# Optimization experiments

Hardware: AMD Instinct MI355X
Metric: run time of the kernel (lower is better)

The kernel has to match this reference:

```python
import jax, jax.numpy as jnp
import numpy as np

N = 100_000   # nodes
E = 1_250_000 # edges
D = 64        # node feature dim
H = 64        # hidden_channels
C = 10        # num_classes
G = 128       # graphs in batch


def setup_inputs() -> dict:
    key = jax.random.key(0)
    ks = jax.random.split(key, 12)
    x = jax.random.normal(ks[0], (N, D), dtype=jnp.float32)
    edge_index = jax.random.randint(ks[1], (2, E), 0, N, dtype=jnp.int64)
    batch = jnp.sort(jax.random.randint(ks[2], (N,), 0, G, dtype=jnp.int64))
    s = lambda fan_in: 1.0 / np.sqrt(fan_in)
    W1 = jax.random.normal(ks[3], (D, H), dtype=jnp.float32) * s(D)
    b1 = jnp.zeros((H,), dtype=jnp.float32)
    W2 = jax.random.normal(ks[4], (H, H), dtype=jnp.float32) * s(H)
    b2 = jnp.zeros((H,), dtype=jnp.float32)
    W3 = jax.random.normal(ks[5], (H, H), dtype=jnp.float32) * s(H)
    b3 = jnp.zeros((H,), dtype=jnp.float32)
    Wl = jax.random.normal(ks[6], (H, C), dtype=jnp.float32) * s(H)
    bl = jnp.zeros((C,), dtype=jnp.float32)
    return {"x": x, "edge_index": edge_index, "batch": batch,
            "W1": W1, "b1": b1, "W2": W2, "b2": b2,
            "W3": W3, "b3": b3, "Wl": Wl, "bl": bl}


def _gcn_conv(h, W, b, src, dst, norm, n_nodes):
    # GCNConv: out[i] = sum_{e: dst(e)=i} norm_e * (h @ W)[src(e)] + b
    h = h @ W
    msg = h[src] * norm[:, None]                       # [E+N, H]
    return jax.ops.segment_sum(msg, dst, num_segments=n_nodes) + b


def reference(x, edge_index, batch, W1, b1, W2, b2, W3, b3, Wl, bl):
    x = x.astype(jnp.float32)
    ei = edge_index.astype(jnp.int64)
    # add self-loops (as PyG gcn_norm does by default)
    loop = jnp.arange(N, dtype=ei.dtype)
    src = jnp.concatenate([ei[0], loop])
    dst = jnp.concatenate([ei[1], loop])
    # symmetric normalization: deg over targets (in-degree incl. self-loops)
    deg = jax.ops.segment_sum(jnp.ones_like(src, dtype=jnp.float32), dst,
                              num_segments=N)
    dinv = jnp.where(deg > 0, jax.lax.rsqrt(jnp.maximum(deg, 1.0)), 0.0)
    norm = dinv[src] * dinv[dst]                       # [E+N]

    h = jax.nn.relu(_gcn_conv(x, W1, b1, src, dst, norm, N))
    h = jax.nn.relu(_gcn_conv(h, W2, b2, src, dst, norm, N))
    h = _gcn_conv(h, W3, b3, src, dst, norm, N)

    # global_mean_pool over graph ids
    ones = jnp.ones((N,), dtype=jnp.float32)
    counts = jax.ops.segment_sum(ones, batch, num_segments=G)
    sums = jax.ops.segment_sum(h, batch, num_segments=G)
    pooled = sums / jnp.maximum(counts, 1.0)[:, None]  # [G, H]

    # dropout is identity in eval mode
    return pooled @ Wl + bl                            # [G, C]
```

## Files before the change

### kernel.cpp

```cpp
#include <hip/hip_runtime.h>
#include <hip/hip_bf16.h>


#define BSHIFT 7
#define BNODES (1 << BSHIFT)
#define EPB    8192
#define MAXDEG 8192
#define MAXBUCKET 32768

typedef __attribute__((ext_vector_type(8))) short bf16x8;
typedef __attribute__((ext_vector_type(4))) float f32x4;

#define KAS __attribute__((address_space(4)))

template <typename T>
__device__ __forceinline__ const KAS T* kptr(const T* p) {
    return (const KAS T*)(unsigned long long)p;
}

__device__ __forceinline__ void atomAddF(float* p, float v) {
#if defined(__gfx90a__) || defined(__gfx940__) || defined(__gfx941__) || defined(__gfx942__) || defined(__gfx950__)
    unsafeAtomicAdd(p, v);
#else
    atomicAdd(p, v);
#endif
}

__device__ __forceinline__ unsigned short f2bf(float x) {
    unsigned u = __float_as_uint(x);
    u += 0x7FFFu + ((u >> 16) & 1u);
    return (unsigned short)(u >> 16);
}
__device__ __forceinline__ float bf2f(unsigned short b) {
    return __uint_as_float((unsigned)b << 16);
}

__global__ __launch_bounds__(256)
void k_bhist(const int* __restrict__ dst, int* __restrict__ cnt_all,
             int nE, int nBuckets, int binBlocks,
             const float* __restrict__ W1, const float* __restrict__ W2,
             const float* __restrict__ W3, unsigned short* __restrict__ Wt,
             float* __restrict__ pool, int poolN) {
    if (blockIdx.x >= binBlocks) {
        int li = blockIdx.x - binBlocks;
        if (li < 3) {
            const float* W = (li == 0) ? W1 : ((li == 1) ? W2 : W3);
            unsigned short* o = Wt + li * 4096;
            for (int idx = threadIdx.x; idx < 4096; idx += 256) {
                int h = idx >> 6, k = idx & 63;
                o[idx] = f2bf(W[k * 64 + h]);
            }
        } else {
            for (int i = threadIdx.x; i < poolN; i += 256) pool[i] = 0.f;
        }
        return;
    }
    __shared__ int cnt[1024];
    const int t = threadIdx.x;
    const int blk = blockIdx.x * EPB;
    for (int b = t; b < nBuckets; b += 256) cnt[b] = 0;
    __syncthreads();
#pragma unroll 4
    for (int i = 0; i < EPB / 256; i++) {
        int e = blk + i * 256 + t;
        if (e < nE) atomicAdd(&cnt[dst[e] >> BSHIFT], 1);
    }
    __syncthreads();
    for (int b = t; b < nBuckets; b += 256)
        cnt_all[(size_t)blockIdx.x * nBuckets + b] = cnt[b];
}

__global__ __launch_bounds__(256)
void k_colscan(int* __restrict__ cnt_all, int* __restrict__ bcnt,
               int nBlocks, int nBuckets) {
    const int lane = threadIdx.x & 63;
    const int b = blockIdx.x * 4 + (threadIdx.x >> 6);
    if (b >= nBuckets) return;
    int running = 0;
    for (int c = 0; c < nBlocks; c += 64) {
        int blk = c + lane;
        int v = (blk < nBlocks) ? cnt_all[(size_t)blk * nBuckets + b] : 0;
        int incl = v;
#pragma unroll
        for (int off = 1; off < 64; off <<= 1) {
            int tv = __shfl_up(incl, off);
            if (lane >= off) incl += tv;
        }
        if (blk < nBlocks) cnt_all[(size_t)blk * nBuckets + b] = running + (incl - v);
        running += __shfl(incl, 63);
    }
    if (lane == 0) bcnt[b] = running;
}

__global__ void k_bscan(const int* __restrict__ bcnt, int* __restrict__ bbase,
                        int nb, int nE) {
    __shared__ int s[256];
    const int t = threadIdx.x;
    const int base = t * 4;
    int v0 = (base + 0 < nb) ? bcnt[base + 0] : 0;
    int v1 = (base + 1 < nb) ? bcnt[base + 1] : 0;
    int v2 = (base + 2 < nb) ? bcnt[base + 2] : 0;
    int v3 = (base + 3 < nb) ? bcnt[base + 3] : 0;
    int tsum = v0 + v1 + v2 + v3;
    s[t] = tsum;
    __syncthreads();
    for (int off = 1; off < 256; off <<= 1) {
        int val = 0;
        if (t >= off) val = s[t - off];
        __syncthreads();
        if (t >= off) s[t] += val;
        __syncthreads();
    }
    int excl = s[t] - tsum;
    if (base + 0 < nb) bbase[base + 0] = excl;
    if (base + 1 < nb) bbase[base + 1] = excl + v0;
    if (base + 2 < nb) bbase[base + 2] = excl + v0 + v1;
    if (base + 3 < nb) bbase[base + 3] = excl + v0 + v1 + v2;
    if (t == 0) bbase[nb] = nE;
}

__global__ __launch_bounds__(256)
void k_bucket(const int* __restrict__ src, const int* __restrict__ dst,
              const int* __restrict__ bbase, const int* __restrict__ cnt_all,
              int* __restrict__ staging, int nE, int nBuckets) {
    __shared__ int cnt[1024];
    __shared__ int lbase[1024];
    const int t = threadIdx.x;
    const int blk = blockIdx.x * EPB;

    for (int b = t; b < nBuckets; b += 256) {
        lbase[b] = bbase[b] + cnt_all[(size_t)blockIdx.x * nBuckets + b];
        cnt[b] = 0;
    }
    __syncthreads();
#pragma unroll 4
    for (int i = 0; i < EPB / 256; i++) {
        int e = blk + i * 256 + t;
        if (e < nE) {
            int s0 = src[e], d0 = dst[e];
            int b = d0 >> BSHIFT;
            int off = atomicAdd(&cnt[b], 1);
            int pos = lbase[b] + off;
            if ((unsigned)pos < (unsigned)nE)
                staging[pos] = (s0 << BSHIFT) | (d0 & (BNODES - 1));
        }
    }
}

__global__ __launch_bounds__(256)
void k_sort(const int* __restrict__ staging, const int* __restrict__ bbase,
            int* __restrict__ csr_s, int* __restrict__ rowptr,
            int* __restrict__ rowend, float* __restrict__ dinv,
            int n, int nE) {
    __shared__ int c[BNODES];
    __shared__ int sc[BNODES];
    __shared__ int cur[BNODES];
    const int t = threadIdx.x;
    const int b = blockIdx.x;
    const int node0 = b << BSHIFT;

    int seg0 = bbase[b];
    int seg1 = bbase[b + 1];
    seg0 = max(0, min(seg0, nE));
    seg1 = max(seg0, min(seg1, nE));
    seg1 = min(seg1, seg0 + MAXBUCKET);

    if (t < BNODES) c[t] = 0;
    __syncthreads();
    for (int e = seg0 + t; e < seg1; e += 256)
        atomicAdd(&c[staging[e] & (BNODES - 1)], 1);
    __syncthreads();
    if (t < BNODES) sc[t] = c[t];
    __syncthreads();
    for (int off = 1; off < BNODES; off <<= 1) {
        int v = 0;
        if (t >= off && t < BNODES) v = sc[t - off];
        __syncthreads();
        if (t >= off && t < BNODES) sc[t] += v;
        __syncthreads();
    }
    if (t < BNODES) {
        int excl = sc[t] - c[t];
        cur[t] = excl;
        int node = node0 + t;
        if (node < n) {
            rowptr[node] = seg0 + excl;
            rowend[node] = seg0 + excl + c[t];
            dinv[node]   = rsqrtf((float)c[t] + 1.0f);
        }
    }
    __syncthreads();
    for (int e = seg0 + t; e < seg1; e += 256) {
        int p = staging[e];
        int l = p & (BNODES - 1);
        int pos = seg0 + atomicAdd(&cur[l], 1);
        if ((unsigned)pos < (unsigned)nE)
            csr_s[pos] = ((unsigned)p) >> BSHIFT;
    }
}

template<bool RELU, typename AT>
__device__ __forceinline__
void gemm_body(int bid, const AT* __restrict__ in,
               const unsigned short* __restrict__ Wt,
               const float* __restrict__ bias,
               unsigned short* __restrict__ out, int n) {
    const int lane = threadIdx.x & 63;
    const int wid  = threadIdx.x >> 6;
    const int col  = lane & 15;
    const int quad = lane >> 4;
    const int node0w = bid * 64 + wid * 16;
    const int nodeA  = node0w + col;
    const bool validA = nodeA < n;

    f32x4 zero4 = {0.f, 0.f, 0.f, 0.f};
    f32x4 acc0 = zero4, acc1 = zero4, acc2 = zero4, acc3 = zero4;

#pragma unroll
    for (int ks = 0; ks < 64; ks += 32) {
        const int kb = ks + quad * 8;
        float a[8];
        if constexpr (sizeof(AT) == 4) {
            float4 a0 = make_float4(0.f, 0.f, 0.f, 0.f);
            float4 a1 = make_float4(0.f, 0.f, 0.f, 0.f);
            if (validA) {
                a0 = *(const float4*)((const float*)in + (size_t)nodeA * 64 + kb);
                a1 = *(const float4*)((const float*)in + (size_t)nodeA * 64 + kb + 4);
            }
            a[0] = a0.x; a[1] = a0.y; a[2] = a0.z; a[3] = a0.w;
            a[4] = a1.x; a[5] = a1.y; a[6] = a1.z; a[7] = a1.w;
        } else {
            ushort4 h0 = make_ushort4(0, 0, 0, 0), h1 = make_ushort4(0, 0, 0, 0);
            if (validA) {
                h0 = *(const ushort4*)((const unsigned short*)in + (size_t)nodeA * 64 + kb);
                h1 = *(const ushort4*)((const unsigned short*)in + (size_t)nodeA * 64 + kb + 4);
            }
            a[0] = bf2f(h0.x); a[1] = bf2f(h0.y); a[2] = bf2f(h0.z); a[3] = bf2f(h0.w);
            a[4] = bf2f(h1.x); a[5] = bf2f(h1.y); a[6] = bf2f(h1.z); a[7] = bf2f(h1.w);
        }
        if (RELU) {
#pragma unroll
            for (int i = 0; i < 8; i++) a[i] = fmaxf(a[i] + bias[kb + i], 0.f);
        }
        bf16x8 af;
#pragma unroll
        for (int i = 0; i < 8; i++) af[i] = (short)f2bf(a[i]);

        const bf16x8 b0f = *(const bf16x8*)(Wt + ((0 * 16 + col) * 64 + kb));
        const bf16x8 b1f = *(const bf16x8*)(Wt + ((1 * 16 + col) * 64 + kb));
        const bf16x8 b2f = *(const bf16x8*)(Wt + ((2 * 16 + col) * 64 + kb));
        const bf16x8 b3f = *(const bf16x8*)(Wt + ((3 * 16 + col) * 64 + kb));
        acc0 = __builtin_amdgcn_mfma_f32_16x16x32_bf16(af, b0f, acc0, 0, 0, 0);
        acc1 = __builtin_amdgcn_mfma_f32_16x16x32_bf16(af, b1f, acc1, 0, 0, 0);
        acc2 = __builtin_amdgcn_mfma_f32_16x16x32_bf16(af, b2f, acc2, 0, 0, 0);
        acc3 = __builtin_amdgcn_mfma_f32_16x16x32_bf16(af, b3f, acc3, 0, 0, 0);
    }

#pragma unroll
    for (int r = 0; r < 4; r++) {
        int nn = node0w + quad * 4 + r;
        if (nn < n) {
            size_t base = (size_t)nn * 64 + col;
            out[base +  0] = f2bf(acc0[r]);
            out[base + 16] = f2bf(acc1[r]);
            out[base + 32] = f2bf(acc2[r]);
            out[base + 48] = f2bf(acc3[r]);
        }
    }
}

template<bool RELU, typename AT>
__global__ __launch_bounds__(256)
void k_gemm(const AT* __restrict__ in, const unsigned short* __restrict__ Wt,
            const float* __restrict__ bias, unsigned short* __restrict__ out, int n) {
    gemm_body<RELU, AT>(blockIdx.x, in, Wt, bias, out, n);
}

__global__ __launch_bounds__(256)
void k_wfgemm1(const int* __restrict__ csr_s, const float* __restrict__ dinv,
               float* __restrict__ csr_w, int nE, int n, int wfB,
               const float* __restrict__ x, const unsigned short* __restrict__ Wt,
               unsigned short* __restrict__ hW) {
    if (blockIdx.x < wfB) {
        int e = blockIdx.x * 256 + threadIdx.x;
        if (e < nE) {
            int s = csr_s[e];
            s = max(0, min(s, n - 1));
            csr_w[e] = dinv[s];
        }
        return;
    }
    gemm_body<false, float>(blockIdx.x - wfB, x, Wt, nullptr, hW, n);
}

template<int LAYER>
__global__ __launch_bounds__(256)
void k_agg(const unsigned short* __restrict__ hW, const int* __restrict__ rowptr,
           const int* __restrict__ rowend, const int* __restrict__ csr_s,
           const float* __restrict__ csr_w, const float* __restrict__ dinv,
           unsigned short* __restrict__ aggb, int n, int nE) {
    const int lane = threadIdx.x & 63;
    const int wid  = threadIdx.x >> 6;
    const int node = blockIdx.x * 4 + wid;
    if (node >= n) return;

    int rowA = __builtin_amdgcn_readfirstlane(rowptr[node]);
    int endA = __builtin_amdgcn_readfirstlane(rowend[node]);
    rowA = max(0, min(rowA, nE)); endA = max(rowA, min(endA, nE));
    endA = min(endA, rowA + MAXDEG);
    const float diA = __uint_as_float(
        __builtin_amdgcn_readfirstlane(__float_as_uint(dinv[node])));

    float acc0 = diA * bf2f(hW[(size_t)node * 64 + lane]);
    float acc1 = 0.f, acc2 = 0.f, acc3 = 0.f;
    const int nm1 = n - 1;

    for (int b = rowA; b < endA; b += 16) {
        const KAS int*   sp = kptr(csr_s + b);
        const KAS float* wp = kptr(csr_w + b);
        const int rem = endA - b;

        int   sidx[16];
        float w[16];
#pragma unroll
        for (int j = 0; j < 16; j++) {
            int s = sp[j];
            s = max(0, min(s, nm1));
            sidx[j] = (j < rem) ? s : 0;
            w[j]    = (j < rem) ? wp[j] : 0.f;
        }
        float h[16];
#pragma unroll
        for (int j = 0; j < 16; j++)
            h[j] = bf2f(hW[(size_t)sidx[j] * 64 + lane]);
#pragma unroll
        for (int j = 0; j < 16; j += 4) {
            acc0 += w[j]     * h[j];
            acc1 += w[j + 1] * h[j + 1];
            acc2 += w[j + 2] * h[j + 2];
            acc3 += w[j + 3] * h[j + 3];
        }
    }
    float r = diA * ((acc0 + acc1) + (acc2 + acc3));
    aggb[(size_t)node * 64 + lane] = f2bf(r);
}

__global__ void k_pool(const unsigned short* __restrict__ aggb,
                       const int* __restrict__ batch,
                       float* __restrict__ pool, float* __restrict__ cnt, int n) {
    const int lane = threadIdx.x;
    const int base = blockIdx.x * 64;
    int g_cur = -1, run = 0;
    float acc = 0.f;
    for (int j = 0; j < 64; j++) {
        int node = base + j;
        if (node >= n) break;
        int g = batch[node];
        if (g != g_cur) {
            if (g_cur >= 0) {
                atomAddF(&pool[g_cur * 64 + lane], acc);
                if (lane == 0) atomAddF(&cnt[g_cur], (float)run);
            }
            g_cur = g; acc = 0.f; run = 0;
        }
        acc += bf2f(aggb[(size_t)node * 64 + lane]);
        run++;
    }
    if (g_cur >= 0) {
        atomAddF(&pool[g_cur * 64 + lane], acc);
        if (lane == 0) atomAddF(&cnt[g_cur], (float)run);
    }
}

__global__ void k_final(const float* __restrict__ pool, const float* __restrict__ cnt,
                        const float* __restrict__ b3, const float* __restrict__ Wl,
                        const float* __restrict__ bl, float* __restrict__ out) {
    __shared__ float s[64];
    const int g = blockIdx.x, t = threadIdx.x;
    float c = fmaxf(cnt[g], 1.0f);
    s[t] = pool[g * 64 + t] / c + b3[t];
    __syncthreads();
    if (t < 10) {
        float acc = bl[t];
#pragma unroll
        for (int k = 0; k < 64; k++) acc += s[k] * Wl[k * 10 + t];
        out[g * 10 + t] = acc;
    }
}

extern "C" void kernel_launch(void* const* d_in, const int* in_sizes, int n_in,
                              void* d_out, int out_size, void* d_ws, size_t ws_size,
                              hipStream_t stream) {
    const float* x   = (const float*)d_in[0];
    const int*   ei  = (const int*)d_in[1];
    const int*   bat = (const int*)d_in[2];
    const float* W1  = (const float*)d_in[3];
    const float* b1  = (const float*)d_in[4];
    const float* W2  = (const float*)d_in[5];
    const float* b2  = (const float*)d_in[6];
    const float* W3  = (const float*)d_in[7];
    const float* b3  = (const float*)d_in[8];
    const float* Wl  = (const float*)d_in[9];
    const float* bl  = (const float*)d_in[10];
    float* out = (float*)d_out;

    const int N_ = in_sizes[0] / 64;
    const int E_ = in_sizes[1] / 2;
    const int G_ = out_size / 10;
    const int NB_ = (N_ + BNODES - 1) >> BSHIFT;
    const int bin_blocks = (E_ + EPB - 1) / EPB;

    char* p = (char*)d_ws;
    int*   staging = (int*)p;   p += (size_t)E_ * 4;
    int*   csr_s  = (int*)p;    p += (size_t)E_ * 4;
    float* csr_w  = (float*)p;  p += (size_t)E_ * 4;
    unsigned short* aggb = (unsigned short*)p; p += (size_t)N_ * 64 * 2;
    unsigned short* hW   = (unsigned short*)p; p += (size_t)N_ * 64 * 2;
    float* dinv   = (float*)p;  p += (size_t)N_ * 4;
    int*   rowptr = (int*)p;    p += (size_t)N_ * 4;
    int*   rowend = (int*)p;    p += (size_t)N_ * 4;
    float* pool   = (float*)p;  p += (size_t)G_ * 64 * 4;
    float* cnt    = (float*)p;  p += (size_t)G_ * 4;
    unsigned short* Wt = (unsigned short*)p; p += 3 * 4096 * 2;
    int*   bcnt   = (int*)p;    p += (size_t)(NB_ + 1) * 4;
    int*   bbase  = (int*)p;    p += (size_t)(NB_ + 1) * 4;
    int*   cnt_all = (int*)p;   p += (size_t)bin_blocks * NB_ * 4;

    const int* srcp = ei;
    const int* dstp = ei + E_;

    k_bhist<<<bin_blocks + 4, 256, 0, stream>>>(dstp, cnt_all, E_, NB_,
                                                bin_blocks, W1, W2, W3, Wt,
                                                pool, G_ * 64 + G_);
    k_colscan<<<(NB_ + 3) / 4, 256, 0, stream>>>(cnt_all, bcnt, bin_blocks, NB_);
    k_bscan<<<1, 256, 0, stream>>>(bcnt, bbase, NB_, E_);
    k_bucket<<<bin_blocks, 256, 0, stream>>>(srcp, dstp, bbase, cnt_all,
                                             staging, E_, NB_);
    k_sort<<<NB_, 256, 0, stream>>>(staging, bbase, csr_s, rowptr, rowend,
                                    dinv, N_, E_);

    const int gemm_blocks = (N_ + 63) / 64;
    const int agg_blocks  = (N_ + 3) / 4;
    const int wf_blocks   = (E_ + 255) / 256;

    k_wfgemm1<<<wf_blocks + gemm_blocks, 256, 0, stream>>>(
        csr_s, dinv, csr_w, E_, N_, wf_blocks, x, Wt, hW);
    k_agg<1><<<agg_blocks, 256, 0, stream>>>(hW, rowptr, rowend, csr_s, csr_w,
                                             dinv, aggb, N_, E_);
    k_gemm<true, unsigned short><<<gemm_blocks, 256, 0, stream>>>(aggb, Wt + 4096,
                                                                  b1, hW, N_);
    k_agg<2><<<agg_blocks, 256, 0, stream>>>(hW, rowptr, rowend, csr_s, csr_w,
                                             dinv, aggb, N_, E_);
    k_gemm<true, unsigned short><<<gemm_blocks, 256, 0, stream>>>(aggb, Wt + 8192,
                                                                  b2, hW, N_);
    k_agg<3><<<agg_blocks, 256, 0, stream>>>(hW, rowptr, rowend, csr_s, csr_w,
                                             dinv, aggb, N_, E_);

    k_pool<<<(N_ + 63) / 64, 64, 0, stream>>>(aggb, bat, pool, cnt, N_);
    k_final<<<G_, 64, 0, stream>>>(pool, cnt, b3, Wl, bl, out);
}
```

Before: 363.5 us.

## Restructure aggregation to 8 edges per wave with 16-byte vector row loads

The aggregation kernel now splits each wavefront into 8 groups of 8 lanes. Each group handles one edge per step and each lane loads 8 bf16 features as one 16-byte vector, where before all 64 lanes walked the same edge one feature per lane. This widens memory transactions and lets each wave keep more independent edge gathers in flight. The cost is a cross-lane shuffle reduction at the end. The scalar-broadcast edge index and weight loads also become per-lane vector loads, adding instruction overhead.

```diff
diff --git a/kernel.cpp b/kernel.cpp
--- a/kernel.cpp
+++ b/kernel.cpp
@@ -10,13 +10,7 @@
 
 typedef __attribute__((ext_vector_type(8))) short bf16x8;
 typedef __attribute__((ext_vector_type(4))) float f32x4;
-
-#define KAS __attribute__((address_space(4)))
-
-template <typename T>
-__device__ __forceinline__ const KAS T* kptr(const T* p) {
-    return (const KAS T*)(unsigned long long)p;
-}
+typedef __attribute__((ext_vector_type(8))) unsigned short u16x8;
 
 __device__ __forceinline__ void atomAddF(float* p, float v) {
 #if defined(__gfx90a__) || defined(__gfx940__) || defined(__gfx941__) || defined(__gfx942__) || defined(__gfx950__)
@@ -299,50 +293,55 @@
            const int* __restrict__ rowend, const int* __restrict__ csr_s,
            const float* __restrict__ csr_w, const float* __restrict__ dinv,
            unsigned short* __restrict__ aggb, int n, int nE) {
-    const int lane = threadIdx.x & 63;
-    const int wid  = threadIdx.x >> 6;
-    const int node = blockIdx.x * 4 + wid;
+    const int lane  = threadIdx.x & 63;
+    const int wid   = threadIdx.x >> 6;
+    const int node  = blockIdx.x * 4 + wid;
     if (node >= n) return;
-
-    int rowA = __builtin_amdgcn_readfirstlane(rowptr[node]);
-    int endA = __builtin_amdgcn_readfirstlane(rowend[node]);
+    const int g     = lane >> 3;
+    const int dslot = lane & 7;
+
+    int rowA = rowptr[node], endA = rowend[node];
     rowA = max(0, min(rowA, nE)); endA = max(rowA, min(endA, nE));
     endA = min(endA, rowA + MAXDEG);
-    const float diA = __uint_as_float(
-        __builtin_amdgcn_readfirstlane(__float_as_uint(dinv[node])));
-
-    float acc0 = diA * bf2f(hW[(size_t)node * 64 + lane]);
-    float acc1 = 0.f, acc2 = 0.f, acc3 = 0.f;
+    const float diA = dinv[node];
     const int nm1 = n - 1;
 
+    float acc[8];
+#pragma unroll
+    for (int i = 0; i < 8; i++) acc[i] = 0.f;
+
     for (int b = rowA; b < endA; b += 16) {
-        const KAS int*   sp = kptr(csr_s + b);
-        const KAS float* wp = kptr(csr_w + b);
-        const int rem = endA - b;
-
-        int   sidx[16];
-        float w[16];
-#pragma unroll
-        for (int j = 0; j < 16; j++) {
-            int s = sp[j];
-            s = max(0, min(s, nm1));
-            sidx[j] = (j < rem) ? s : 0;
-            w[j]    = (j < rem) ? wp[j] : 0.f;
-        }
-        float h[16];
-#pragma unroll
-        for (int j = 0; j < 16; j++)
-            h[j] = bf2f(hW[(size_t)sidx[j] * 64 + lane]);
-#pragma unroll
-        for (int j = 0; j < 16; j += 4) {
-            acc0 += w[j]     * h[j];
-            acc1 += w[j + 1] * h[j + 1];
-            acc2 += w[j + 2] * h[j + 2];
-            acc3 += w[j + 3] * h[j + 3];
-        }
-    }
-    float r = diA * ((acc0 + acc1) + (acc2 + acc3));
-    aggb[(size_t)node * 64 + lane] = f2bf(r);
+        const int e0 = b + g;
+        const int e1 = b + 8 + g;
+        int   s0 = 0, s1 = 0;
+        float w0 = 0.f, w1 = 0.f;
+        if (e0 < endA) { s0 = csr_s[e0]; w0 = csr_w[e0]; }
+        if (e1 < endA) { s1 = csr_s[e1]; w1 = csr_w[e1]; }
+        s0 = max(0, min(s0, nm1));
+        s1 = max(0, min(s1, nm1));
+        const u16x8 h0 = *(const u16x8*)(hW + (size_t)s0 * 64 + dslot * 8);
+        const u16x8 h1 = *(const u16x8*)(hW + (size_t)s1 * 64 + dslot * 8);
+#pragma unroll
+        for (int i = 0; i < 8; i++) {
+            acc[i] += w0 * bf2f(h0[i]);
+            acc[i] += w1 * bf2f(h1[i]);
+        }
+    }
+
+#pragma unroll
+    for (int off = 8; off < 64; off <<= 1) {
+#pragma unroll
+        for (int i = 0; i < 8; i++) acc[i] += __shfl_xor(acc[i], off);
+    }
+
+    if (g == 0) {
+        const u16x8 hs = *(const u16x8*)(hW + (size_t)node * 64 + dslot * 8);
+        u16x8 r;
+#pragma unroll
+        for (int i = 0; i < 8; i++)
+            r[i] = f2bf(diA * (acc[i] + diA * bf2f(hs[i])));
+        *(u16x8*)(aggb + (size_t)node * 64 + dslot * 8) = r;
+    }
 }
 
 __global__ void k_pool(const unsigned short* __restrict__ aggb,
```

After: 349.4 us. -3.9%, faster.
